# Kernel optimization log

Hardware: AMD Instinct MI355X
Metric: run time of the kernel (lower is better)

Reference implementation:

```python
import jax, jax.numpy as jnp
import numpy as np

D_IN = 64   # T (condition_length)
D = 128     # latent_dim
H = 8       # num_head
N = 2       # batch of graphs
M = 512     # num_nodes
T_OBS = 5.0


def leaky(v):
    return jnp.where(v >= 0, v, 0.2 * v)


def setup_inputs() -> dict:
    key = jax.random.key(0)
    ks = jax.random.split(key, 24)
    g = lambda k, s: jax.random.normal(k, s, dtype=jnp.float32) * 0.05
    return {
        "x": jax.random.normal(ks[0], (N, M, D_IN), dtype=jnp.float32),
        # f_node: T -> 2D -> D
        "fn_w1": g(ks[1], (D_IN, 2 * D)), "fn_b1": g(ks[2], (2 * D,)),
        "fn_w2": g(ks[3], (2 * D, D)),   "fn_b2": g(ks[4], (D,)),
        # per-head K/Q/V projections, stacked over heads
        "wk": g(ks[5], (H, D, D)), "bk": g(ks[6], (H, D)),
        "wq": g(ks[7], (H, D, D)), "bq": g(ks[8], (H, D)),
        "wv": g(ks[9], (H, D, D)), "bv": g(ks[10], (H, D)),
        # f_v: H*D -> D -> D
        "fv_w1": g(ks[11], (H * D, D)), "fv_b1": g(ks[12], (D,)),
        "fv_w2": g(ks[13], (D, D)),     "fv_b2": g(ks[14], (D,)),
        # f_node2edge: 2D -> D -> 1
        "fe_w1": g(ks[15], (2 * D, D)), "fe_b1": g(ks[16], (D,)),
        "fe_w2": g(ks[17], (D, 1)),     "fe_b2": g(ks[18], (1,)),
    }


def reference(x, fn_w1, fn_b1, fn_w2, fn_b2, wk, bk, wq, bq, wv, bv,
              fv_w1, fv_b1, fv_w2, fv_b2, fe_w1, fe_b1, fe_w2, fe_b2):
    n, m, T = x.shape
    # TemporalEncoding with d_hid=1: div_term = [1.0], even col -> sin(t)
    t = jnp.linspace(0.0, T_OBS, T)
    te = jnp.sin(t)  # [T]
    # f_node
    h = jax.nn.relu((x + te) @ fn_w1 + fn_b1) @ fn_w2 + fn_b2  # [N,M,D]
    # per-head attention (sender=K_i, receiver=Q_j -> scores = K Q^T)
    K = jnp.einsum('nmd,hde->hnme', h, wk) + bk[:, None, None, :]
    Q = jnp.einsum('nmd,hde->hnme', h, wq) + bq[:, None, None, :]
    V = jnp.einsum('nmd,hde->hnme', h, wv) + bv[:, None, None, :]
    scores = jnp.einsum('hnid,hnjd->hnij', K, Q)           # [H,N,M,M]
    alpha = jax.nn.softmax(leaky(scores), axis=-1)
    att = leaky(jnp.einsum('hnij,hnjd->hnid', alpha, V))   # [H,N,M,D]
    # concat heads along feature dim (head 0 first)
    att = jnp.transpose(att, (1, 2, 0, 3)).reshape(n, m, -1)  # [N,M,H*D]
    x2 = jax.nn.relu(att @ fv_w1 + fv_b1) @ fv_w2 + fv_b2 + h  # [N,M,D]
    # pairwise node2edge FFN: pair(i,j) = concat(x2_i, x2_j)
    half = fe_w1.shape[0] // 2
    A = x2 @ fe_w1[:half]   # contribution of node i
    B = x2 @ fe_w1[half:]   # contribution of node j
    hid = jax.nn.relu(A[:, :, None, :] + B[:, None, :, :] + fe_b1)  # [N,M,M,D]
    edge = (hid @ fe_w2 + fe_b2)[..., 0] / float(m)  # [N,M,M]
    return (x2, edge)
```

## Files before the change

kernel.cpp:

```cpp
#include <hip/hip_runtime.h>

typedef unsigned short u16;
typedef unsigned int u32;
typedef __attribute__((ext_vector_type(8))) short short8;
typedef __attribute__((ext_vector_type(4))) float f32x4;

__device__ __forceinline__ u16 f2b(float f) {
  union { float f; u32 i; } v; v.f = f;
  u32 i = v.i;
  return (u16)((i + 0x7FFFu + ((i >> 16) & 1u)) >> 16);
}
__device__ __forceinline__ float lo16(u32 x) { union { u32 i; float f; } v; v.i = x << 16; return v.f; }
__device__ __forceinline__ float hi16(u32 x) { union { u32 i; float f; } v; v.i = x & 0xffff0000u; return v.f; }
__device__ __forceinline__ u32 pack2(float a, float b) { return (u32)f2b(a) | ((u32)f2b(b) << 16); }

__device__ __align__(16) float g_h[1024 * 128];
__device__ __align__(16) u16   g_K[16 * 512 * 128];
__device__ __align__(16) u16   g_Q[16 * 512 * 128];
__device__ __align__(16) u16   g_V[16 * 512 * 128];
__device__ __align__(16) float g_Op[512 * 64 * 128];
__device__ __align__(16) float g_ml[512 * 64 * 2];
__device__ __align__(16) u16   g_att[1024 * 1024];
__device__ __align__(16) float g_part[2 * 1024 * 128];
__device__ __align__(16) float g_A[1024 * 128];
__device__ __align__(16) float g_Bm[1024 * 128];

__global__ void k_fnode(const float* __restrict__ x, const float* __restrict__ w1,
                        const float* __restrict__ b1, const float* __restrict__ w2,
                        const float* __restrict__ b2) {
  __shared__ float xr[2 * 64];
  __shared__ float hids[2 * 256];
  __shared__ float red[2048];
  int tx = threadIdx.x;
  int row0 = blockIdx.x * 2;
  if (tx < 128) {
    int r = tx >> 6, k = tx & 63;
    xr[tx] = x[(row0 + r) * 64 + k] + sinf((float)k * (5.0f / 63.0f));
  }
  __syncthreads();
  {
    int ks = tx >> 6, cg = tx & 63;
    float acc[2][4] = {};
#pragma unroll 4
    for (int i = 0; i < 16; i++) {
      int k = ks * 16 + i;
      float4 w4 = *(const float4*)&w1[k * 256 + cg * 4];
      float a0 = xr[k], a1 = xr[64 + k];
      acc[0][0] = fmaf(a0, w4.x, acc[0][0]); acc[0][1] = fmaf(a0, w4.y, acc[0][1]);
      acc[0][2] = fmaf(a0, w4.z, acc[0][2]); acc[0][3] = fmaf(a0, w4.w, acc[0][3]);
      acc[1][0] = fmaf(a1, w4.x, acc[1][0]); acc[1][1] = fmaf(a1, w4.y, acc[1][1]);
      acc[1][2] = fmaf(a1, w4.z, acc[1][2]); acc[1][3] = fmaf(a1, w4.w, acc[1][3]);
    }
#pragma unroll
    for (int r = 0; r < 2; r++)
      *(float4*)&red[ks * 512 + r * 256 + cg * 4] = *(float4*)acc[r];
  }
  __syncthreads();
#pragma unroll
  for (int jo = 0; jo < 2; jo++) {
    int o = jo * 256 + tx;
    float s = red[o] + red[512 + o] + red[1024 + o] + red[1536 + o];
    hids[o] = fmaxf(s + b1[o & 255], 0.0f);
  }
  __syncthreads();
  {
    int ks = tx >> 5, eg = tx & 31;
    float acc[2][4] = {};
#pragma unroll 4
    for (int i = 0; i < 32; i++) {
      int k = ks * 32 + i;
      float4 w4 = *(const float4*)&w2[k * 128 + eg * 4];
      float a0 = hids[k], a1 = hids[256 + k];
      acc[0][0] = fmaf(a0, w4.x, acc[0][0]); acc[0][1] = fmaf(a0, w4.y, acc[0][1]);
      acc[0][2] = fmaf(a0, w4.z, acc[0][2]); acc[0][3] = fmaf(a0, w4.w, acc[0][3]);
      acc[1][0] = fmaf(a1, w4.x, acc[1][0]); acc[1][1] = fmaf(a1, w4.y, acc[1][1]);
      acc[1][2] = fmaf(a1, w4.z, acc[1][2]); acc[1][3] = fmaf(a1, w4.w, acc[1][3]);
    }
    __syncthreads();
#pragma unroll
    for (int r = 0; r < 2; r++)
      *(float4*)&red[ks * 256 + r * 128 + eg * 4] = *(float4*)acc[r];
  }
  __syncthreads();
  {
    float s = 0.0f;
#pragma unroll
    for (int ks = 0; ks < 8; ks++) s += red[ks * 256 + tx];
    int r = tx >> 7, e = tx & 127;
    g_h[(row0 + r) * 128 + e] = s + b2[e];
  }
}

__global__ void k_kqv(const float* __restrict__ wk, const float* __restrict__ bk,
                      const float* __restrict__ wq, const float* __restrict__ bq,
                      const float* __restrict__ wv, const float* __restrict__ bv) {
  int b = blockIdx.x, tx = threadIdx.x;
  int ct = b % 48, rt = b / 48;
  int c0 = ct * 64;
  int proj = c0 >> 10, rem = c0 & 1023, head = rem >> 7, e0 = rem & 127;
  const float* W  = (proj == 0) ? wk : (proj == 1) ? wq : wv;
  const float* Bb = (proj == 0) ? bk : (proj == 1) ? bq : bv;
  u16* O = (proj == 0) ? g_K : (proj == 1) ? g_Q : g_V;
  __shared__ float hs[64 * 132];
  __shared__ float wt[64 * 68];
  int r0 = rt * 64;
#pragma unroll
  for (int t = 0; t < 32; t++) {
    int idx = t * 256 + tx, r = idx >> 7, d = idx & 127;
    hs[r * 132 + d] = g_h[(r0 + r) * 128 + d];
  }
  int rg = tx >> 4, cg = tx & 15;
  float acc[4][4] = {};
  const float* Wh = W + head * 16384 + e0;
  for (int kk = 0; kk < 128; kk += 64) {
    __syncthreads();
#pragma unroll
    for (int t = 0; t < 16; t++) {
      int idx = t * 256 + tx, k = idx >> 6, j = idx & 63;
      wt[k * 68 + j] = Wh[(kk + k) * 128 + j];
    }
    __syncthreads();
    const float* hrow = &hs[(rg * 4) * 132 + kk];
#pragma unroll 4
    for (int d4 = 0; d4 < 64; d4 += 4) {
      float4 a[4];
      a[0] = *(const float4*)&hrow[d4];
      a[1] = *(const float4*)&hrow[132 + d4];
      a[2] = *(const float4*)&hrow[264 + d4];
      a[3] = *(const float4*)&hrow[396 + d4];
      float4 w0 = *(const float4*)&wt[(d4 + 0) * 68 + cg * 4];
      float4 w1v = *(const float4*)&wt[(d4 + 1) * 68 + cg * 4];
      float4 w2v = *(const float4*)&wt[(d4 + 2) * 68 + cg * 4];
      float4 w3v = *(const float4*)&wt[(d4 + 3) * 68 + cg * 4];
#pragma unroll
      for (int ri = 0; ri < 4; ri++) {
        acc[ri][0] = fmaf(a[ri].x, w0.x, acc[ri][0]);
        acc[ri][1] = fmaf(a[ri].x, w0.y, acc[ri][1]);
        acc[ri][2] = fmaf(a[ri].x, w0.z, acc[ri][2]);
        acc[ri][3] = fmaf(a[ri].x, w0.w, acc[ri][3]);
        acc[ri][0] = fmaf(a[ri].y, w1v.x, acc[ri][0]);
        acc[ri][1] = fmaf(a[ri].y, w1v.y, acc[ri][1]);
        acc[ri][2] = fmaf(a[ri].y, w1v.z, acc[ri][2]);
        acc[ri][3] = fmaf(a[ri].y, w1v.w, acc[ri][3]);
        acc[ri][0] = fmaf(a[ri].z, w2v.x, acc[ri][0]);
        acc[ri][1] = fmaf(a[ri].z, w2v.y, acc[ri][1]);
        acc[ri][2] = fmaf(a[ri].z, w2v.z, acc[ri][2]);
        acc[ri][3] = fmaf(a[ri].z, w2v.w, acc[ri][3]);
        acc[ri][0] = fmaf(a[ri].w, w3v.x, acc[ri][0]);
        acc[ri][1] = fmaf(a[ri].w, w3v.y, acc[ri][1]);
        acc[ri][2] = fmaf(a[ri].w, w3v.z, acc[ri][2]);
        acc[ri][3] = fmaf(a[ri].w, w3v.w, acc[ri][3]);
      }
    }
  }
#pragma unroll
  for (int ri = 0; ri < 4; ri++) {
    int grow = r0 + rg * 4 + ri;
    int eb = e0 + cg * 4;
    float v0 = acc[ri][0] + Bb[head * 128 + eb + 0];
    float v1 = acc[ri][1] + Bb[head * 128 + eb + 1];
    float v2 = acc[ri][2] + Bb[head * 128 + eb + 2];
    float v3 = acc[ri][3] + Bb[head * 128 + eb + 3];
    uint2 st = make_uint2(pack2(v0, v1), pack2(v2, v3));
    *(uint2*)&O[(head * 1024 + grow) * 128 + eb] = st;
  }
}

__global__ __launch_bounds__(256) void k_attn() {
  __shared__ u16 Ks[64 * 136];
  __shared__ u16 Qs[64 * 136];
  __shared__ u16 Vt[128 * 72];
  __shared__ u16 Pw[4 * 16 * 72];
  __shared__ float alphas[4 * 16];
  int b = blockIdx.x, tx = threadIdx.x;
  int jc = b & 3, it = (b >> 2) & 7, hn = b >> 5;
  int i0 = it * 64;
  const u16* Kp = g_K + hn * 65536;
  const u16* Qp = g_Q + hn * 65536;
  const u16* Vp = g_V + hn * 65536;
#pragma unroll
  for (int t = 0; t < 4; t++) {
    int idx = t * 256 + tx, row = idx >> 4, oct = idx & 15;
    *(uint4*)&Ks[row * 136 + oct * 8] = *(const uint4*)&Kp[(i0 + row) * 128 + oct * 8];
  }
  int lane = tx & 63, wv = tx >> 6;
  int cl = lane & 15, quad = lane >> 4;
  f32x4 zero = {0.0f, 0.0f, 0.0f, 0.0f};
  f32x4 o[8];
#pragma unroll
  for (int es = 0; es < 8; es++) o[es] = zero;
  float m_ = -1e30f, l_ = 0.0f;

  for (int jt = 0; jt < 2; jt++) {
    int j0 = jc * 128 + jt * 64;
    __syncthreads();
#pragma unroll
    for (int t = 0; t < 4; t++) {
      int idx = t * 256 + tx, row = idx >> 4, oct = idx & 15;
      *(uint4*)&Qs[row * 136 + oct * 8] = *(const uint4*)&Qp[(j0 + row) * 128 + oct * 8];
    }
    {
      int jg = (tx & 15) * 4, e8 = (tx >> 4) * 8;
      uint4 r0 = *(const uint4*)&Vp[(j0 + jg + 0) * 128 + e8];
      uint4 r1 = *(const uint4*)&Vp[(j0 + jg + 1) * 128 + e8];
      uint4 r2 = *(const uint4*)&Vp[(j0 + jg + 2) * 128 + e8];
      uint4 r3 = *(const uint4*)&Vp[(j0 + jg + 3) * 128 + e8];
      const u32* p0 = (const u32*)&r0; const u32* p1 = (const u32*)&r1;
      const u32* p2 = (const u32*)&r2; const u32* p3 = (const u32*)&r3;
#pragma unroll
      for (int c = 0; c < 8; c++) {
        int w = c >> 1, sh = (c & 1) * 16;
        u32 lo = ((p0[w] >> sh) & 0xffffu) | (((p1[w] >> sh) & 0xffffu) << 16);
        u32 hi = ((p2[w] >> sh) & 0xffffu) | (((p3[w] >> sh) & 0xffffu) << 16);
        *(uint2*)&Vt[(e8 + c) * 72 + jg] = make_uint2(lo, hi);
      }
    }
    __syncthreads();
    short8 bK[4];
#pragma unroll
    for (int kk = 0; kk < 4; kk++)
      bK[kk] = *(const short8*)&Ks[(wv * 16 + cl) * 136 + kk * 32 + quad * 8];
    f32x4 st[4];
#pragma unroll
    for (int s = 0; s < 4; s++) {
      f32x4 acc = zero;
#pragma unroll
      for (int kk = 0; kk < 4; kk++) {
        short8 aQ = *(const short8*)&Qs[(s * 16 + cl) * 136 + kk * 32 + quad * 8];
        acc = __builtin_amdgcn_mfma_f32_16x16x32_bf16(aQ, bK[kk], acc, 0, 0, 0);
      }
      st[s] = acc;
    }
    float p[4][4];
    float tm = -1e30f;
#pragma unroll
    for (int s = 0; s < 4; s++)
#pragma unroll
      for (int r = 0; r < 4; r++) {
        float v = st[s][r];
        v = fmaxf(v, 0.2f * v);
        p[s][r] = v;
        tm = fmaxf(tm, v);
      }
    tm = fmaxf(tm, __shfl_xor(tm, 16));
    tm = fmaxf(tm, __shfl_xor(tm, 32));
    float mn = fmaxf(m_, tm);
    float alpha = __expf(m_ - mn);
    m_ = mn;
    float ps = 0.0f;
#pragma unroll
    for (int s = 0; s < 4; s++)
#pragma unroll
      for (int r = 0; r < 4; r++) {
        float e = __expf(p[s][r] - mn);
        p[s][r] = e;
        ps += e;
      }
    ps += __shfl_xor(ps, 16);
    ps += __shfl_xor(ps, 32);
    l_ = l_ * alpha + ps;
#pragma unroll
    for (int s = 0; s < 4; s++) {
      uint2 w2v = make_uint2(pack2(p[s][0], p[s][1]), pack2(p[s][2], p[s][3]));
      *(uint2*)&Pw[(wv * 16 + cl) * 72 + s * 16 + quad * 4] = w2v;
    }
    if (quad == 0) alphas[wv * 16 + cl] = alpha;
    __syncthreads();
    f32x4 av = *(const f32x4*)&alphas[wv * 16 + quad * 4];
#pragma unroll
    for (int es = 0; es < 8; es++) o[es] *= av;
    short8 aP[2];
#pragma unroll
    for (int k2 = 0; k2 < 2; k2++)
      aP[k2] = *(const short8*)&Pw[(wv * 16 + cl) * 72 + k2 * 32 + quad * 8];
#pragma unroll
    for (int es = 0; es < 8; es++) {
#pragma unroll
      for (int k2 = 0; k2 < 2; k2++) {
        short8 bV = *(const short8*)&Vt[(es * 16 + cl) * 72 + k2 * 32 + quad * 8];
        o[es] = __builtin_amdgcn_mfma_f32_16x16x32_bf16(aP[k2], bV, o[es], 0, 0, 0);
      }
    }
  }
#pragma unroll
  for (int es = 0; es < 8; es++)
#pragma unroll
    for (int r = 0; r < 4; r++)
      g_Op[(b * 64 + wv * 16 + quad * 4 + r) * 128 + es * 16 + cl] = o[es][r];
  if (quad == 0) {
    g_ml[(b * 64 + wv * 16 + cl) * 2 + 0] = m_;
    g_ml[(b * 64 + wv * 16 + cl) * 2 + 1] = l_;
  }
}

__global__ void k_amerge() {
  int b = blockIdx.x, tx = threadIdx.x;
  int hn = b >> 5, ig = b & 31;
  int row = ig * 16 + (tx >> 4);
  int c8 = (tx & 15) * 8;
  int it = row >> 6, lr = row & 63;
  float mc[4], lc[4];
  float4 oa[4], ob[4];
#pragma unroll
  for (int c = 0; c < 4; c++) {
    int bp = hn * 32 + it * 4 + c;
    float2 ml = *(const float2*)&g_ml[(bp * 64 + lr) * 2];
    mc[c] = ml.x; lc[c] = ml.y;
    oa[c] = *(const float4*)&g_Op[(bp * 64 + lr) * 128 + c8];
    ob[c] = *(const float4*)&g_Op[(bp * 64 + lr) * 128 + c8 + 4];
  }
  float ms = fmaxf(fmaxf(mc[0], mc[1]), fmaxf(mc[2], mc[3]));
  float lsum = 0.0f;
  float ra[8] = {};
#pragma unroll
  for (int c = 0; c < 4; c++) {
    float w = __expf(mc[c] - ms);
    lsum += w * lc[c];
    ra[0] = fmaf(w, oa[c].x, ra[0]); ra[1] = fmaf(w, oa[c].y, ra[1]);
    ra[2] = fmaf(w, oa[c].z, ra[2]); ra[3] = fmaf(w, oa[c].w, ra[3]);
    ra[4] = fmaf(w, ob[c].x, ra[4]); ra[5] = fmaf(w, ob[c].y, ra[5]);
    ra[6] = fmaf(w, ob[c].z, ra[6]); ra[7] = fmaf(w, ob[c].w, ra[7]);
  }
  float inv = 1.0f / lsum;
  u16 pk[8];
#pragma unroll
  for (int e = 0; e < 8; e++) {
    float v = ra[e] * inv;
    v = fmaxf(v, 0.2f * v);
    pk[e] = f2b(v);
  }
  int h = hn >> 1, n = hn & 1;
  uint4 st;
  st.x = (u32)pk[0] | ((u32)pk[1] << 16);
  st.y = (u32)pk[2] | ((u32)pk[3] << 16);
  st.z = (u32)pk[4] | ((u32)pk[5] << 16);
  st.w = (u32)pk[6] | ((u32)pk[7] << 16);
  *(uint4*)&g_att[(n * 512 + row) * 1024 + h * 128 + c8] = st;
}

__global__ void k_fv1(const float* __restrict__ w1) {
  __shared__ float atts[4 * 512];
  __shared__ float red[8 * 512];
  int b = blockIdx.x, tx = threadIdx.x;
  int row0 = (b >> 1) * 4, kh = b & 1, k0 = kh * 512;
#pragma unroll
  for (int j = 0; j < 8; j++) {
    int idx = j * 256 + tx, r = idx >> 9, c = idx & 511;
    atts[r * 512 + c] = lo16((u32)g_att[(row0 + r) * 1024 + k0 + c]);
  }
  __syncthreads();
  int ks = tx >> 5, eg = tx & 31;
  float acc[4][4] = {};
  int kbase = k0 + ks * 64;
#pragma unroll 4
  for (int i = 0; i < 64; i++) {
    int k = kbase + i;
    float4 w4 = *(const float4*)&w1[k * 128 + eg * 4];
    int kl = ks * 64 + i;
    float a0 = atts[kl], a1 = atts[512 + kl], a2 = atts[1024 + kl], a3 = atts[1536 + kl];
    acc[0][0] = fmaf(a0, w4.x, acc[0][0]); acc[0][1] = fmaf(a0, w4.y, acc[0][1]);
    acc[0][2] = fmaf(a0, w4.z, acc[0][2]); acc[0][3] = fmaf(a0, w4.w, acc[0][3]);
    acc[1][0] = fmaf(a1, w4.x, acc[1][0]); acc[1][1] = fmaf(a1, w4.y, acc[1][1]);
    acc[1][2] = fmaf(a1, w4.z, acc[1][2]); acc[1][3] = fmaf(a1, w4.w, acc[1][3]);
    acc[2][0] = fmaf(a2, w4.x, acc[2][0]); acc[2][1] = fmaf(a2, w4.y, acc[2][1]);
    acc[2][2] = fmaf(a2, w4.z, acc[2][2]); acc[2][3] = fmaf(a2, w4.w, acc[2][3]);
    acc[3][0] = fmaf(a3, w4.x, acc[3][0]); acc[3][1] = fmaf(a3, w4.y, acc[3][1]);
    acc[3][2] = fmaf(a3, w4.z, acc[3][2]); acc[3][3] = fmaf(a3, w4.w, acc[3][3]);
  }
#pragma unroll
  for (int r = 0; r < 4; r++)
    *(float4*)&red[ks * 512 + r * 128 + eg * 4] = *(float4*)acc[r];
  __syncthreads();
#pragma unroll
  for (int jo = 0; jo < 2; jo++) {
    int o = jo * 256 + tx;
    float s = 0.0f;
#pragma unroll
    for (int k8 = 0; k8 < 8; k8++) s += red[k8 * 512 + o];
    int r = o >> 7, e = o & 127;
    g_part[kh * 131072 + (row0 + r) * 128 + e] = s;
  }
}

__global__ void k_fv2(const float* __restrict__ b1, const float* __restrict__ w2,
                      const float* __restrict__ b2, const float* __restrict__ few1,
                      const float* __restrict__ feb1, float* __restrict__ x2out) {
  __shared__ float hids[2 * 128];
  __shared__ float x2s[2 * 128];
  __shared__ float red[8 * 256];
  int b = blockIdx.x, tx = threadIdx.x;
  int row0 = b * 2;
  {
    int r = tx >> 7, e = tx & 127;
    int gi = (row0 + r) * 128 + e;
    float s = g_part[gi] + g_part[131072 + gi] + b1[e];
    hids[tx] = fmaxf(s, 0.0f);
  }
  __syncthreads();
  int ks = tx >> 5, eg = tx & 31;
  {
    float acc[2][4] = {};
#pragma unroll 4
    for (int i = 0; i < 16; i++) {
      int k = ks * 16 + i;
      float4 w4 = *(const float4*)&w2[k * 128 + eg * 4];
      float a0 = hids[k], a1 = hids[128 + k];
      acc[0][0] = fmaf(a0, w4.x, acc[0][0]); acc[0][1] = fmaf(a0, w4.y, acc[0][1]);
      acc[0][2] = fmaf(a0, w4.z, acc[0][2]); acc[0][3] = fmaf(a0, w4.w, acc[0][3]);
      acc[1][0] = fmaf(a1, w4.x, acc[1][0]); acc[1][1] = fmaf(a1, w4.y, acc[1][1]);
      acc[1][2] = fmaf(a1, w4.z, acc[1][2]); acc[1][3] = fmaf(a1, w4.w, acc[1][3]);
    }
#pragma unroll
    for (int r = 0; r < 2; r++)
      *(float4*)&red[ks * 256 + r * 128 + eg * 4] = *(float4*)acc[r];
  }
  __syncthreads();
  {
    float s = 0.0f;
#pragma unroll
    for (int k8 = 0; k8 < 8; k8++) s += red[k8 * 256 + tx];
    int r = tx >> 7, e = tx & 127;
    int gi = (row0 + r) * 128 + e;
    float c = s + b2[e] + g_h[gi];
    x2s[tx] = c;
    x2out[gi] = c;
  }
  __syncthreads();
  float aA[2][4] = {}, aB[2][4] = {};
#pragma unroll 4
  for (int i = 0; i < 16; i++) {
    int k = ks * 16 + i;
    float4 wa = *(const float4*)&few1[k * 128 + eg * 4];
    float4 wb = *(const float4*)&few1[(128 + k) * 128 + eg * 4];
    float a0 = x2s[k], a1 = x2s[128 + k];
    aA[0][0] = fmaf(a0, wa.x, aA[0][0]); aA[0][1] = fmaf(a0, wa.y, aA[0][1]);
    aA[0][2] = fmaf(a0, wa.z, aA[0][2]); aA[0][3] = fmaf(a0, wa.w, aA[0][3]);
    aA[1][0] = fmaf(a1, wa.x, aA[1][0]); aA[1][1] = fmaf(a1, wa.y, aA[1][1]);
    aA[1][2] = fmaf(a1, wa.z, aA[1][2]); aA[1][3] = fmaf(a1, wa.w, aA[1][3]);
    aB[0][0] = fmaf(a0, wb.x, aB[0][0]); aB[0][1] = fmaf(a0, wb.y, aB[0][1]);
    aB[0][2] = fmaf(a0, wb.z, aB[0][2]); aB[0][3] = fmaf(a0, wb.w, aB[0][3]);
    aB[1][0] = fmaf(a1, wb.x, aB[1][0]); aB[1][1] = fmaf(a1, wb.y, aB[1][1]);
    aB[1][2] = fmaf(a1, wb.z, aB[1][2]); aB[1][3] = fmaf(a1, wb.w, aB[1][3]);
  }
  __syncthreads();
#pragma unroll
  for (int r = 0; r < 2; r++)
    *(float4*)&red[ks * 256 + r * 128 + eg * 4] = *(float4*)aA[r];
  __syncthreads();
  {
    float s = 0.0f;
#pragma unroll
    for (int k8 = 0; k8 < 8; k8++) s += red[k8 * 256 + tx];
    int r = tx >> 7, e = tx & 127;
    g_A[(row0 + r) * 128 + e] = s + feb1[e];
  }
  __syncthreads();
#pragma unroll
  for (int r = 0; r < 2; r++)
    *(float4*)&red[ks * 256 + r * 128 + eg * 4] = *(float4*)aB[r];
  __syncthreads();
  {
    float s = 0.0f;
#pragma unroll
    for (int k8 = 0; k8 < 8; k8++) s += red[k8 * 256 + tx];
    int r = tx >> 7, e = tx & 127;
    g_Bm[(row0 + r) * 128 + e] = s;
  }
}

__global__ void k_edge(const float* __restrict__ few2, const float* __restrict__ feb2,
                       float* __restrict__ edge) {
  __shared__ float As[4 * 128];
  __shared__ float w2s[128];
  int b = blockIdx.x, tx = threadIdx.x;
  int n = b >> 8, rest = b & 255, ig = rest >> 1, jh = rest & 1;
  int i0 = ig * 4;
  if (tx < 128) w2s[tx] = few2[tx];
  As[tx] = g_A[(n * 512 + i0) * 128 + tx];
  As[tx + 256] = g_A[(n * 512 + i0) * 128 + tx + 256];
  float eb2 = feb2[0];
  __syncthreads();
  int j = jh * 256 + tx;
  const float* B0 = &g_Bm[(n * 512 + j) * 128];
  float acc[4] = {};
#pragma unroll 4
  for (int dc = 0; dc < 32; dc++) {
    float4 bv = *(const float4*)&B0[dc * 4];
    float4 w4 = *(const float4*)&w2s[dc * 4];
#pragma unroll
    for (int i = 0; i < 4; i++) {
      float4 a4 = *(const float4*)&As[i * 128 + dc * 4];
      acc[i] = fmaf(fmaxf(a4.x + bv.x, 0.0f), w4.x, acc[i]);
      acc[i] = fmaf(fmaxf(a4.y + bv.y, 0.0f), w4.y, acc[i]);
      acc[i] = fmaf(fmaxf(a4.z + bv.z, 0.0f), w4.z, acc[i]);
      acc[i] = fmaf(fmaxf(a4.w + bv.w, 0.0f), w4.w, acc[i]);
    }
  }
  const float scale = 1.0f / 512.0f;
#pragma unroll
  for (int i = 0; i < 4; i++)
    edge[(n * 512 + i0 + i) * 512 + j] = (acc[i] + eb2) * scale;
}

extern "C" void kernel_launch(void* const* d_in, const int* in_sizes, int n_in,
                              void* d_out, int out_size, void* d_ws, size_t ws_size,
                              hipStream_t stream) {
  (void)in_sizes; (void)n_in; (void)out_size; (void)d_ws; (void)ws_size;
  const float* x     = (const float*)d_in[0];
  const float* fn_w1 = (const float*)d_in[1];
  const float* fn_b1 = (const float*)d_in[2];
  const float* fn_w2 = (const float*)d_in[3];
  const float* fn_b2 = (const float*)d_in[4];
  const float* wk    = (const float*)d_in[5];
  const float* bk    = (const float*)d_in[6];
  const float* wq    = (const float*)d_in[7];
  const float* bq    = (const float*)d_in[8];
  const float* wv    = (const float*)d_in[9];
  const float* bv    = (const float*)d_in[10];
  const float* fv_w1 = (const float*)d_in[11];
  const float* fv_b1 = (const float*)d_in[12];
  const float* fv_w2 = (const float*)d_in[13];
  const float* fv_b2 = (const float*)d_in[14];
  const float* fe_w1 = (const float*)d_in[15];
  const float* fe_b1 = (const float*)d_in[16];
  const float* fe_w2 = (const float*)d_in[17];
  const float* fe_b2 = (const float*)d_in[18];

  float* x2out = (float*)d_out;
  float* edge  = x2out + 131072;

  k_fnode<<<512, 256, 0, stream>>>(x, fn_w1, fn_b1, fn_w2, fn_b2);
  k_kqv<<<768, 256, 0, stream>>>(wk, bk, wq, bq, wv, bv);
  k_attn<<<512, 256, 0, stream>>>();
  k_amerge<<<512, 256, 0, stream>>>();
  k_fv1<<<512, 256, 0, stream>>>(fv_w1);
  k_fv2<<<512, 256, 0, stream>>>(fv_b1, fv_w2, fv_b2, fe_w1, fe_b1, x2out);
  k_edge<<<512, 256, 0, stream>>>(fe_w2, fe_b2, edge);
}
```

Measured before the change: 162.6 us.

## Use bf16 MFMA for KQV projection and fv1 GEMM

Rewrites the K/Q/V projection and the first f_v layer as bf16 MFMA 16x16x32 GEMMs. Weights are converted and transposed into LDS per block, and f_node now also writes a bf16 copy of h. fv1 splits K into 8 chunks whose fp32 partials k_fv2 sums, replacing the previous 2-way split. This aims to cut scalar FMA cost, trading it for bf16 rounding of h and the fv1 weights plus extra partial-buffer traffic.

Result: faster. 148.7 us (-8.5%).

```diff
diff --git a/kernel.cpp b/kernel.cpp
--- a/kernel.cpp
+++ b/kernel.cpp
@@ -15,13 +15,14 @@
 __device__ __forceinline__ u32 pack2(float a, float b) { return (u32)f2b(a) | ((u32)f2b(b) << 16); }
 
 __device__ __align__(16) float g_h[1024 * 128];
+__device__ __align__(16) u16   g_hb[1024 * 128];
 __device__ __align__(16) u16   g_K[16 * 512 * 128];
 __device__ __align__(16) u16   g_Q[16 * 512 * 128];
 __device__ __align__(16) u16   g_V[16 * 512 * 128];
 __device__ __align__(16) float g_Op[512 * 64 * 128];
 __device__ __align__(16) float g_ml[512 * 64 * 2];
 __device__ __align__(16) u16   g_att[1024 * 1024];
-__device__ __align__(16) float g_part[2 * 1024 * 128];
+__device__ __align__(16) float g_part8[8 * 1024 * 128];
 __device__ __align__(16) float g_A[1024 * 128];
 __device__ __align__(16) float g_Bm[1024 * 128];
 
@@ -87,82 +88,73 @@
 #pragma unroll
     for (int ks = 0; ks < 8; ks++) s += red[ks * 256 + tx];
     int r = tx >> 7, e = tx & 127;
-    g_h[(row0 + r) * 128 + e] = s + b2[e];
-  }
-}
-
-__global__ void k_kqv(const float* __restrict__ wk, const float* __restrict__ bk,
-                      const float* __restrict__ wq, const float* __restrict__ bq,
-                      const float* __restrict__ wv, const float* __restrict__ bv) {
+    float v = s + b2[e];
+    g_h[(row0 + r) * 128 + e] = v;
+    g_hb[(row0 + r) * 128 + e] = f2b(v);
+  }
+}
+
+__global__ __launch_bounds__(256) void k_kqv(
+    const float* __restrict__ wk, const float* __restrict__ bk,
+    const float* __restrict__ wq, const float* __restrict__ bq,
+    const float* __restrict__ wv, const float* __restrict__ bv) {
+  __shared__ u16 hs[64 * 136];
+  __shared__ u16 Wt[128 * 136];
   int b = blockIdx.x, tx = threadIdx.x;
-  int ct = b % 48, rt = b / 48;
-  int c0 = ct * 64;
-  int proj = c0 >> 10, rem = c0 & 1023, head = rem >> 7, e0 = rem & 127;
+  int rt = b & 15, ph = b >> 4;
+  int proj = ph >> 3, head = ph & 7;
   const float* W  = (proj == 0) ? wk : (proj == 1) ? wq : wv;
   const float* Bb = (proj == 0) ? bk : (proj == 1) ? bq : bv;
   u16* O = (proj == 0) ? g_K : (proj == 1) ? g_Q : g_V;
-  __shared__ float hs[64 * 132];
-  __shared__ float wt[64 * 68];
   int r0 = rt * 64;
 #pragma unroll
-  for (int t = 0; t < 32; t++) {
-    int idx = t * 256 + tx, r = idx >> 7, d = idx & 127;
-    hs[r * 132 + d] = g_h[(r0 + r) * 128 + d];
-  }
-  int rg = tx >> 4, cg = tx & 15;
-  float acc[4][4] = {};
-  const float* Wh = W + head * 16384 + e0;
-  for (int kk = 0; kk < 128; kk += 64) {
-    __syncthreads();
-#pragma unroll
-    for (int t = 0; t < 16; t++) {
-      int idx = t * 256 + tx, k = idx >> 6, j = idx & 63;
-      wt[k * 68 + j] = Wh[(kk + k) * 128 + j];
-    }
-    __syncthreads();
-    const float* hrow = &hs[(rg * 4) * 132 + kk];
-#pragma unroll 4
-    for (int d4 = 0; d4 < 64; d4 += 4) {
-      float4 a[4];
-      a[0] = *(const float4*)&hrow[d4];
-      a[1] = *(const float4*)&hrow[132 + d4];
-      a[2] = *(const float4*)&hrow[264 + d4];
-      a[3] = *(const float4*)&hrow[396 + d4];
-      float4 w0 = *(const float4*)&wt[(d4 + 0) * 68 + cg * 4];
-      float4 w1v = *(const float4*)&wt[(d4 + 1) * 68 + cg * 4];
-      float4 w2v = *(const float4*)&wt[(d4 + 2) * 68 + cg * 4];
-      float4 w3v = *(const float4*)&wt[(d4 + 3) * 68 + cg * 4];
-#pragma unroll
-      for (int ri = 0; ri < 4; ri++) {
-        acc[ri][0] = fmaf(a[ri].x, w0.x, acc[ri][0]);
-        acc[ri][1] = fmaf(a[ri].x, w0.y, acc[ri][1]);
-        acc[ri][2] = fmaf(a[ri].x, w0.z, acc[ri][2]);
-        acc[ri][3] = fmaf(a[ri].x, w0.w, acc[ri][3]);
-        acc[ri][0] = fmaf(a[ri].y, w1v.x, acc[ri][0]);
-        acc[ri][1] = fmaf(a[ri].y, w1v.y, acc[ri][1]);
-        acc[ri][2] = fmaf(a[ri].y, w1v.z, acc[ri][2]);
-        acc[ri][3] = fmaf(a[ri].y, w1v.w, acc[ri][3]);
-        acc[ri][0] = fmaf(a[ri].z, w2v.x, acc[ri][0]);
-        acc[ri][1] = fmaf(a[ri].z, w2v.y, acc[ri][1]);
-        acc[ri][2] = fmaf(a[ri].z, w2v.z, acc[ri][2]);
-        acc[ri][3] = fmaf(a[ri].z, w2v.w, acc[ri][3]);
-        acc[ri][0] = fmaf(a[ri].w, w3v.x, acc[ri][0]);
-        acc[ri][1] = fmaf(a[ri].w, w3v.y, acc[ri][1]);
-        acc[ri][2] = fmaf(a[ri].w, w3v.z, acc[ri][2]);
-        acc[ri][3] = fmaf(a[ri].w, w3v.w, acc[ri][3]);
-      }
-    }
-  }
-#pragma unroll
-  for (int ri = 0; ri < 4; ri++) {
-    int grow = r0 + rg * 4 + ri;
-    int eb = e0 + cg * 4;
-    float v0 = acc[ri][0] + Bb[head * 128 + eb + 0];
-    float v1 = acc[ri][1] + Bb[head * 128 + eb + 1];
-    float v2 = acc[ri][2] + Bb[head * 128 + eb + 2];
-    float v3 = acc[ri][3] + Bb[head * 128 + eb + 3];
-    uint2 st = make_uint2(pack2(v0, v1), pack2(v2, v3));
-    *(uint2*)&O[(head * 1024 + grow) * 128 + eb] = st;
+  for (int t = 0; t < 4; t++) {
+    int idx = t * 256 + tx, row = idx >> 4, oct = idx & 15;
+    *(uint4*)&hs[row * 136 + oct * 8] = *(const uint4*)&g_hb[(r0 + row) * 128 + oct * 8];
+  }
+  const float* Wh = W + head * 16384;
+  {
+    int dg = (tx & 31) * 4;
+#pragma unroll
+    for (int half = 0; half < 2; half++) {
+      int e8 = ((tx >> 5) + half * 8) * 8;
+      float rr[4][8];
+#pragma unroll
+      for (int r = 0; r < 4; r++) {
+        float4 a = *(const float4*)&Wh[(dg + r) * 128 + e8];
+        float4 c = *(const float4*)&Wh[(dg + r) * 128 + e8 + 4];
+        rr[r][0] = a.x; rr[r][1] = a.y; rr[r][2] = a.z; rr[r][3] = a.w;
+        rr[r][4] = c.x; rr[r][5] = c.y; rr[r][6] = c.z; rr[r][7] = c.w;
+      }
+#pragma unroll
+      for (int c = 0; c < 8; c++)
+        *(uint2*)&Wt[(e8 + c) * 136 + dg] =
+            make_uint2(pack2(rr[0][c], rr[1][c]), pack2(rr[2][c], rr[3][c]));
+    }
+  }
+  __syncthreads();
+  int lane = tx & 63, wv_ = tx >> 6, cl = lane & 15, quad = lane >> 4;
+  short8 bH[4];
+#pragma unroll
+  for (int kk = 0; kk < 4; kk++)
+    bH[kk] = *(const short8*)&hs[(wv_ * 16 + cl) * 136 + kk * 32 + quad * 8];
+  f32x4 zero = {0.0f, 0.0f, 0.0f, 0.0f};
+  f32x4 acc[8];
+#pragma unroll
+  for (int em = 0; em < 8; em++) acc[em] = zero;
+#pragma unroll
+  for (int em = 0; em < 8; em++)
+#pragma unroll
+    for (int kk = 0; kk < 4; kk++) {
+      short8 aW = *(const short8*)&Wt[(em * 16 + cl) * 136 + kk * 32 + quad * 8];
+      acc[em] = __builtin_amdgcn_mfma_f32_16x16x32_bf16(aW, bH[kk], acc[em], 0, 0, 0);
+    }
+#pragma unroll
+  for (int em = 0; em < 8; em++) {
+    float4 b4 = *(const float4*)&Bb[head * 128 + em * 16 + quad * 4];
+    uint2 st = make_uint2(pack2(acc[em][0] + b4.x, acc[em][1] + b4.y),
+                          pack2(acc[em][2] + b4.z, acc[em][3] + b4.w));
+    *(uint2*)&O[(head * 1024 + r0 + wv_ * 16 + cl) * 128 + em * 16 + quad * 4] = st;
   }
 }
 
@@ -338,48 +330,58 @@
   *(uint4*)&g_att[(n * 512 + row) * 1024 + h * 128 + c8] = st;
 }
 
-__global__ void k_fv1(const float* __restrict__ w1) {
-  __shared__ float atts[4 * 512];
-  __shared__ float red[8 * 512];
+__global__ __launch_bounds__(256) void k_fv1(const float* __restrict__ w1) {
+  __shared__ u16 atts[64 * 136];
+  __shared__ u16 w1t[128 * 136];
   int b = blockIdx.x, tx = threadIdx.x;
-  int row0 = (b >> 1) * 4, kh = b & 1, k0 = kh * 512;
-#pragma unroll
-  for (int j = 0; j < 8; j++) {
-    int idx = j * 256 + tx, r = idx >> 9, c = idx & 511;
-    atts[r * 512 + c] = lo16((u32)g_att[(row0 + r) * 1024 + k0 + c]);
-  }
-  __syncthreads();
-  int ks = tx >> 5, eg = tx & 31;
-  float acc[4][4] = {};
-  int kbase = k0 + ks * 64;
-#pragma unroll 4
-  for (int i = 0; i < 64; i++) {
-    int k = kbase + i;
-    float4 w4 = *(const float4*)&w1[k * 128 + eg * 4];
-    int kl = ks * 64 + i;
-    float a0 = atts[kl], a1 = atts[512 + kl], a2 = atts[1024 + kl], a3 = atts[1536 + kl];
-    acc[0][0] = fmaf(a0, w4.x, acc[0][0]); acc[0][1] = fmaf(a0, w4.y, acc[0][1]);
-    acc[0][2] = fmaf(a0, w4.z, acc[0][2]); acc[0][3] = fmaf(a0, w4.w, acc[0][3]);
-    acc[1][0] = fmaf(a1, w4.x, acc[1][0]); acc[1][1] = fmaf(a1, w4.y, acc[1][1]);
-    acc[1][2] = fmaf(a1, w4.z, acc[1][2]); acc[1][3] = fmaf(a1, w4.w, acc[1][3]);
-    acc[2][0] = fmaf(a2, w4.x, acc[2][0]); acc[2][1] = fmaf(a2, w4.y, acc[2][1]);
-    acc[2][2] = fmaf(a2, w4.z, acc[2][2]); acc[2][3] = fmaf(a2, w4.w, acc[2][3]);
-    acc[3][0] = fmaf(a3, w4.x, acc[3][0]); acc[3][1] = fmaf(a3, w4.y, acc[3][1]);
-    acc[3][2] = fmaf(a3, w4.z, acc[3][2]); acc[3][3] = fmaf(a3, w4.w, acc[3][3]);
-  }
-#pragma unroll
-  for (int r = 0; r < 4; r++)
-    *(float4*)&red[ks * 512 + r * 128 + eg * 4] = *(float4*)acc[r];
-  __syncthreads();
-#pragma unroll
-  for (int jo = 0; jo < 2; jo++) {
-    int o = jo * 256 + tx;
-    float s = 0.0f;
-#pragma unroll
-    for (int k8 = 0; k8 < 8; k8++) s += red[k8 * 512 + o];
-    int r = o >> 7, e = o & 127;
-    g_part[kh * 131072 + (row0 + r) * 128 + e] = s;
-  }
+  int kc = b & 7, rt = b >> 3;
+  int r0 = rt * 64, k0 = kc * 128;
+#pragma unroll
+  for (int t = 0; t < 4; t++) {
+    int idx = t * 256 + tx, row = idx >> 4, oct = idx & 15;
+    *(uint4*)&atts[row * 136 + oct * 8] =
+        *(const uint4*)&g_att[(r0 + row) * 1024 + k0 + oct * 8];
+  }
+  {
+    int dg = (tx & 31) * 4;
+#pragma unroll
+    for (int half = 0; half < 2; half++) {
+      int e8 = ((tx >> 5) + half * 8) * 8;
+      float rr[4][8];
+#pragma unroll
+      for (int r = 0; r < 4; r++) {
+        float4 a = *(const float4*)&w1[(k0 + dg + r) * 128 + e8];
+        float4 c = *(const float4*)&w1[(k0 + dg + r) * 128 + e8 + 4];
+        rr[r][0] = a.x; rr[r][1] = a.y; rr[r][2] = a.z; rr[r][3] = a.w;
+        rr[r][4] = c.x; rr[r][5] = c.y; rr[r][6] = c.z; rr[r][7] = c.w;
+      }
+#pragma unroll
+      for (int c = 0; c < 8; c++)
+        *(uint2*)&w1t[(e8 + c) * 136 + dg] =
+            make_uint2(pack2(rr[0][c], rr[1][c]), pack2(rr[2][c], rr[3][c]));
+    }
+  }
+  __syncthreads();
+  int lane = tx & 63, wv_ = tx >> 6, cl = lane & 15, quad = lane >> 4;
+  short8 bA[4];
+#pragma unroll
+  for (int kk = 0; kk < 4; kk++)
+    bA[kk] = *(const short8*)&atts[(wv_ * 16 + cl) * 136 + kk * 32 + quad * 8];
+  f32x4 zero = {0.0f, 0.0f, 0.0f, 0.0f};
+  f32x4 acc[8];
+#pragma unroll
+  for (int em = 0; em < 8; em++) acc[em] = zero;
+#pragma unroll
+  for (int em = 0; em < 8; em++)
+#pragma unroll
+    for (int kk = 0; kk < 4; kk++) {
+      short8 aW = *(const short8*)&w1t[(em * 16 + cl) * 136 + kk * 32 + quad * 8];
+      acc[em] = __builtin_amdgcn_mfma_f32_16x16x32_bf16(aW, bA[kk], acc[em], 0, 0, 0);
+    }
+#pragma unroll
+  for (int em = 0; em < 8; em++)
+    *(f32x4*)&g_part8[kc * 131072 + (r0 + wv_ * 16 + cl) * 128 + em * 16 + quad * 4] =
+        acc[em];
 }
 
 __global__ void k_fv2(const float* __restrict__ b1, const float* __restrict__ w2,
@@ -393,7 +395,9 @@
   {
     int r = tx >> 7, e = tx & 127;
     int gi = (row0 + r) * 128 + e;
-    float s = g_part[gi] + g_part[131072 + gi] + b1[e];
+    float s = b1[e];
+#pragma unroll
+    for (int kc = 0; kc < 8; kc++) s += g_part8[kc * 131072 + gi];
     hids[tx] = fmaxf(s, 0.0f);
   }
   __syncthreads();
@@ -530,10 +534,10 @@
   float* edge  = x2out + 131072;
 
   k_fnode<<<512, 256, 0, stream>>>(x, fn_w1, fn_b1, fn_w2, fn_b2);
-  k_kqv<<<768, 256, 0, stream>>>(wk, bk, wq, bq, wv, bv);
+  k_kqv<<<384, 256, 0, stream>>>(wk, bk, wq, bq, wv, bv);
   k_attn<<<512, 256, 0, stream>>>();
   k_amerge<<<512, 256, 0, stream>>>();
-  k_fv1<<<512, 256, 0, stream>>>(fv_w1);
+  k_fv1<<<128, 256, 0, stream>>>(fv_w1);
   k_fv2<<<512, 256, 0, stream>>>(fv_b1, fv_w2, fv_b2, fe_w1, fe_b1, x2out);
   k_edge<<<512, 256, 0, stream>>>(fe_w2, fe_b2, edge);
 }
```
